# Kernel optimization log

Hardware: AMD Instinct MI355X
Metric: run time of the kernel (lower is better)

The kernel has to match this reference:

```python
import jax, jax.numpy as jnp
import numpy as np

N_NODES = 50000
N_EDGES = 800000
D = 128
H = 8
DH = D // H  # 16


def setup_inputs() -> dict:
    key = jax.random.key(0)
    ks = jax.random.split(key, 9)
    x = jax.random.normal(ks[0], (N_NODES, D), dtype=jnp.float32)
    # guarantee every node has >=1 incoming edge (avoids z == 0)
    dst_rand = jax.random.randint(ks[1], (N_EDGES - N_NODES,), 0, N_NODES, dtype=jnp.int64 if jax.config.jax_enable_x64 else jnp.int32)
    dst = jnp.concatenate([jnp.arange(N_NODES, dtype=dst_rand.dtype), dst_rand])
    src = jax.random.randint(ks[2], (N_EDGES,), 0, N_NODES, dtype=dst.dtype)
    scale = 0.05
    Wq = jax.random.normal(ks[3], (D, D), dtype=jnp.float32) * scale
    Wk = jax.random.normal(ks[4], (D, D), dtype=jnp.float32) * scale
    Wv = jax.random.normal(ks[5], (D, D), dtype=jnp.float32) * scale
    bq = jax.random.normal(ks[6], (D,), dtype=jnp.float32) * scale
    bk = jax.random.normal(ks[7], (D,), dtype=jnp.float32) * scale
    bv = jax.random.normal(ks[8], (D,), dtype=jnp.float32) * scale
    return {"x": x, "src": src, "dst": dst, "Wq": Wq, "bq": bq, "Wk": Wk, "bk": bk, "Wv": Wv, "bv": bv}


def reference(x, src, dst, Wq, bq, Wk, bk, Wv, bv):
    N = x.shape[0]
    # node projections -> [N, H, DH]
    Q = (x @ Wq + bq).reshape(N, H, DH)
    K = (x @ Wk + bk).reshape(N, H, DH)
    V = (x @ Wv + bv).reshape(N, H, DH)
    scale_const = jnp.sqrt(jnp.float32(DH))
    # per-edge score: (K[src] . Q[dst]) per head, then exp-clamp  -> [E, H]
    score = jnp.einsum('ehd,ehd->eh', K[src], Q[dst])
    score = jnp.exp(jnp.clip(score / scale_const, -5.0, 5.0))
    # scatter-sum by destination node
    wV = jax.ops.segment_sum(score[:, :, None] * V[src], dst, num_segments=N)  # [N,H,DH]
    z = jax.ops.segment_sum(score, dst, num_segments=N)  # [N,H]
    attn = (wV / z[:, :, None]).reshape(N, H * DH)
    # dropout p=0 -> identity; residual
    return x + attn
```

## Files before the change

### kernel.cpp

```cpp
#include <hip/hip_runtime.h>
#include <hip/hip_bf16.h>

#define N_NODES 50000
#define N_EDGES 800000
#define D 128
#define H 8

#define PROJ_BLOCKS ((N_NODES + 63) / 64)
#define HIST_BLOCKS 1024
#define SCAN_T 1024
#define PER_T 50

typedef __attribute__((ext_vector_type(8))) short short8;
typedef __attribute__((ext_vector_type(4))) float floatx4;

__device__ __forceinline__ float bfbits2f(unsigned short u) {
    union { unsigned int i; float f; } c; c.i = ((unsigned int)u) << 16; return c.f;
}
__device__ __forceinline__ unsigned short f2bfbits(float f) {
    __hip_bfloat16 h = __float2bfloat16(f);
    return *reinterpret_cast<unsigned short*>(&h);
}

__global__ __launch_bounds__(256) void prep_w_kernel(
    const float* __restrict__ Wq, const float* __restrict__ Wk,
    const float* __restrict__ Wv, __hip_bfloat16* __restrict__ Wt,
    int* __restrict__ counts)
{
    const int i = blockIdx.x * 256 + threadIdx.x;
    if (i < N_NODES) counts[i] = 0;
    if (i >= 3 * D * D) return;
    const int p = i >> 14;
    const int r = i & (D * D - 1);
    const int col = r >> 7;
    const int k = r & (D - 1);
    const float* W = (p == 0) ? Wq : (p == 1) ? Wk : Wv;
    Wt[i] = __float2bfloat16(W[k * D + col]);
}

__global__ __launch_bounds__(256) void proj_hist_kernel(
    const float* __restrict__ x,
    const __hip_bfloat16* __restrict__ Wt,
    const float* __restrict__ bq, const float* __restrict__ bk,
    const float* __restrict__ bv,
    unsigned short* __restrict__ Qb,
    unsigned int* __restrict__ KVi,
    const int* __restrict__ dst, int* __restrict__ counts)
{
    const int tid = threadIdx.x;

    if (blockIdx.x >= PROJ_BLOCKS) {
        const int i = (blockIdx.x - PROJ_BLOCKS) * 256 + tid;
        const int stride = HIST_BLOCKS * 256;
        for (int e = i; e < N_EDGES; e += stride)
            atomicAdd(&counts[dst[e]], 1);
        return;
    }

    const int m0   = blockIdx.x * 64;
    const int lane = tid & 63;
    const int wv   = tid >> 6;
    const int cb   = wv * 32;
    const int lr   = lane & 15;
    const int hi   = lane >> 4;

    __shared__ short xs[64][136];

    {
        const int row = tid >> 2;
        const int c0  = (tid & 3) * 32;
        int n = m0 + row; if (n >= N_NODES) n = N_NODES - 1;
        const float* xr = x + (size_t)n * D + c0;
        #pragma unroll
        for (int i = 0; i < 8; ++i) {
            const float4 f = *(const float4*)(xr + i * 4);
            short4 s;
            s.x = (short)f2bfbits(f.x); s.y = (short)f2bfbits(f.y);
            s.z = (short)f2bfbits(f.z); s.w = (short)f2bfbits(f.w);
            *(short4*)(&xs[row][c0 + i * 4]) = s;
        }
    }
    __syncthreads();

    floatx4 acc[3][4][2];
    #pragma unroll
    for (int p = 0; p < 3; ++p)
        #pragma unroll
        for (int rt = 0; rt < 4; ++rt)
            #pragma unroll
            for (int ct = 0; ct < 2; ++ct)
                acc[p][rt][ct] = (floatx4){0.f, 0.f, 0.f, 0.f};

    const short* Wts = (const short*)Wt;

    #pragma unroll
    for (int ks = 0; ks < 4; ++ks) {
        const int k0 = ks * 32 + hi * 8;

        short8 bfr[3][2];
        #pragma unroll
        for (int p = 0; p < 3; ++p)
            #pragma unroll
            for (int ct = 0; ct < 2; ++ct) {
                const int col = cb + ct * 16 + lr;
                bfr[p][ct] = *(const short8*)(Wts + ((size_t)(p * D + col) * D + k0));
            }

        short8 afr[4];
        #pragma unroll
        for (int rt = 0; rt < 4; ++rt)
            afr[rt] = *(const short8*)(&xs[rt * 16 + lr][k0]);

        #pragma unroll
        for (int p = 0; p < 3; ++p)
            #pragma unroll
            for (int ct = 0; ct < 2; ++ct)
                #pragma unroll
                for (int rt = 0; rt < 4; ++rt)
                    acc[p][rt][ct] = __builtin_amdgcn_mfma_f32_16x16x32_bf16(
                        afr[rt], bfr[p][ct], acc[p][rt][ct], 0, 0, 0);
    }

    #pragma unroll
    for (int ct = 0; ct < 2; ++ct) {
        const int col = cb + ct * 16 + lr;
        const float bkv = bk[col], bvv = bv[col];
        #pragma unroll
        for (int rt = 0; rt < 4; ++rt) {
            const int node0 = m0 + rt * 16 + hi * 4;
            if (node0 < N_NODES) {
                #pragma unroll
                for (int r = 0; r < 4; ++r) {
                    const unsigned int kk = f2bfbits(acc[1][rt][ct][r] + bkv);
                    const unsigned int vv = f2bfbits(acc[2][rt][ct][r] + bvv);
                    KVi[(size_t)(node0 + r) * 128 + col] = kk | (vv << 16);
                }
            }
        }
    }

    __syncthreads();
    #pragma unroll
    for (int ct = 0; ct < 2; ++ct) {
        const int col = cb + ct * 16 + lr;
        const float bqv = bq[col];
        #pragma unroll
        for (int rt = 0; rt < 4; ++rt) {
            const int nloc = rt * 16 + hi * 4;
            #pragma unroll
            for (int r = 0; r < 4; ++r)
                xs[nloc + r][col] = (short)f2bfbits(acc[0][rt][ct][r] + bqv);
        }
    }
    __syncthreads();
    {
        const int row = tid >> 2;
        const int c0  = (tid & 3) * 32;
        const int n   = m0 + row;
        if (n < N_NODES) {
            int4* dstp = (int4*)(Qb + (size_t)n * D + c0);
            const int4* srcp = (const int4*)(&xs[row][c0]);
            #pragma unroll
            for (int i = 0; i < 4; ++i) dstp[i] = srcp[i];
        }
    }
}

__global__ __launch_bounds__(SCAN_T) void scan_kernel(
    const int* __restrict__ counts, int* __restrict__ row_ptr,
    int* __restrict__ cursor)
{
    __shared__ int wsum[16];
    const int tid  = threadIdx.x;
    const int base = tid * PER_T;

    int tot = 0;
    if (tid < 1000) {
        #pragma unroll 10
        for (int j = 0; j < PER_T; ++j) tot += counts[base + j];
    }

    int incl = tot;
    #pragma unroll
    for (int off = 1; off < 64; off <<= 1) {
        const int v = __shfl_up(incl, off);
        if ((tid & 63) >= off) incl += v;
    }
    if ((tid & 63) == 63) wsum[tid >> 6] = incl;
    __syncthreads();
    if (tid == 0) {
        int run = 0;
        #pragma unroll
        for (int w = 0; w < 16; ++w) { const int v = wsum[w]; wsum[w] = run; run += v; }
    }
    __syncthreads();

    if (tid < 1000) {
        int run = (incl - tot) + wsum[tid >> 6];
        #pragma unroll 10
        for (int j = 0; j < PER_T; ++j) {
            const int c = counts[base + j];
            row_ptr[base + j] = run;
            cursor[base + j]  = run;
            run += c;
        }
    }
    if (tid == 0) row_ptr[N_NODES] = N_EDGES;
}

__global__ __launch_bounds__(256) void scatter_kernel(
    const int* __restrict__ dst, const int* __restrict__ src,
    int* __restrict__ cursor, int* __restrict__ srcs)
{
    const int i = blockIdx.x * blockDim.x + threadIdx.x;
    const int stride = gridDim.x * blockDim.x;
    for (int e = i; e < N_EDGES; e += stride) {
        const int pos = atomicAdd(&cursor[dst[e]], 1);
        srcs[pos] = src[e];
    }
}

__global__ __launch_bounds__(256) void aggregate_kernel(
    const int* __restrict__ row_ptr, const int* __restrict__ srcs,
    const unsigned short* __restrict__ Qb, const unsigned int* __restrict__ KVi,
    const float* __restrict__ x, float* __restrict__ out)
{
    const int lane = threadIdx.x & 63;
    const int t    = (blockIdx.x * blockDim.x + threadIdx.x) >> 6;
    if (t >= N_NODES) return;

    const unsigned int qbits = *(const unsigned int*)(Qb + (size_t)t * D + 2 * lane);
    const float q0 = bfbits2f((unsigned short)(qbits & 0xffff));
    const float q1 = bfbits2f((unsigned short)(qbits >> 16));

    int i = row_ptr[t];
    const int rp1 = row_ptr[t + 1];

    float accx = 0.f, accy = 0.f, zh = 0.f;
    const unsigned long long* KVs = (const unsigned long long*)KVi;

    for (; i + 4 <= rp1; i += 4) {
        const int s0 = srcs[i + 0];
        const int s1 = srcs[i + 1];
        const int s2 = srcs[i + 2];
        const int s3 = srcs[i + 3];
        const unsigned long long kv0 = KVs[(size_t)s0 * 64 + lane];
        const unsigned long long kv1 = KVs[(size_t)s1 * 64 + lane];
        const unsigned long long kv2 = KVs[(size_t)s2 * 64 + lane];
        const unsigned long long kv3 = KVs[(size_t)s3 * 64 + lane];

        float p0 = bfbits2f((unsigned short)kv0) * q0 + bfbits2f((unsigned short)(kv0 >> 32)) * q1;
        float p1 = bfbits2f((unsigned short)kv1) * q0 + bfbits2f((unsigned short)(kv1 >> 32)) * q1;
        float p2 = bfbits2f((unsigned short)kv2) * q0 + bfbits2f((unsigned short)(kv2 >> 32)) * q1;
        float p3 = bfbits2f((unsigned short)kv3) * q0 + bfbits2f((unsigned short)(kv3 >> 32)) * q1;

        p0 += __shfl_xor(p0, 1); p1 += __shfl_xor(p1, 1);
        p2 += __shfl_xor(p2, 1); p3 += __shfl_xor(p3, 1);
        p0 += __shfl_xor(p0, 2); p1 += __shfl_xor(p1, 2);
        p2 += __shfl_xor(p2, 2); p3 += __shfl_xor(p3, 2);
        p0 += __shfl_xor(p0, 4); p1 += __shfl_xor(p1, 4);
        p2 += __shfl_xor(p2, 4); p3 += __shfl_xor(p3, 4);

        const float w0 = __expf(fminf(fmaxf(p0 * 0.25f, -5.0f), 5.0f));
        const float w1 = __expf(fminf(fmaxf(p1 * 0.25f, -5.0f), 5.0f));
        const float w2 = __expf(fminf(fmaxf(p2 * 0.25f, -5.0f), 5.0f));
        const float w3 = __expf(fminf(fmaxf(p3 * 0.25f, -5.0f), 5.0f));

        accx += w0 * bfbits2f((unsigned short)(kv0 >> 16)) + w1 * bfbits2f((unsigned short)(kv1 >> 16))
              + w2 * bfbits2f((unsigned short)(kv2 >> 16)) + w3 * bfbits2f((unsigned short)(kv3 >> 16));
        accy += w0 * bfbits2f((unsigned short)(kv0 >> 48)) + w1 * bfbits2f((unsigned short)(kv1 >> 48))
              + w2 * bfbits2f((unsigned short)(kv2 >> 48)) + w3 * bfbits2f((unsigned short)(kv3 >> 48));
        zh   += (w0 + w1) + (w2 + w3);
    }
    for (; i < rp1; ++i) {
        const int s = srcs[i];
        const unsigned long long kv = KVs[(size_t)s * 64 + lane];
        float p = bfbits2f((unsigned short)kv) * q0 + bfbits2f((unsigned short)(kv >> 32)) * q1;
        p += __shfl_xor(p, 1);
        p += __shfl_xor(p, 2);
        p += __shfl_xor(p, 4);
        const float w = __expf(fminf(fmaxf(p * 0.25f, -5.0f), 5.0f));
        accx += w * bfbits2f((unsigned short)(kv >> 16));
        accy += w * bfbits2f((unsigned short)(kv >> 48));
        zh   += w;
    }

    const float inv = 1.0f / zh;
    const int base = t * D + 2 * lane;
    out[base + 0] = x[base + 0] + accx * inv;
    out[base + 1] = x[base + 1] + accy * inv;
}

extern "C" void kernel_launch(void* const* d_in, const int* in_sizes, int n_in,
                              void* d_out, int out_size, void* d_ws, size_t ws_size,
                              hipStream_t stream) {
    const float* x   = (const float*)d_in[0];
    const int*   src = (const int*)d_in[1];
    const int*   dst = (const int*)d_in[2];
    const float* Wq  = (const float*)d_in[3];
    const float* bq  = (const float*)d_in[4];
    const float* Wk  = (const float*)d_in[5];
    const float* bk  = (const float*)d_in[6];
    const float* Wv  = (const float*)d_in[7];
    const float* bv  = (const float*)d_in[8];

    unsigned short* Qb  = (unsigned short*)d_ws;
    unsigned int*   KVi = (unsigned int*)(Qb + (size_t)N_NODES * D);
    __hip_bfloat16* Wt  = (__hip_bfloat16*)(KVi + (size_t)N_NODES * 128);
    int* counts   = (int*)(Wt + 3 * D * D);
    int* row_ptr  = counts + 50048;
    int* cursor   = row_ptr + 50048;
    int* srcs     = cursor + 50048;

    float* out = (float*)d_out;

    prep_w_kernel<<<196, 256, 0, stream>>>(Wq, Wk, Wv, Wt, counts);

    proj_hist_kernel<<<PROJ_BLOCKS + HIST_BLOCKS, 256, 0, stream>>>(
        x, Wt, bq, bk, bv, Qb, KVi, dst, counts);

    scan_kernel<<<1, SCAN_T, 0, stream>>>(counts, row_ptr, cursor);

    scatter_kernel<<<1024, 256, 0, stream>>>(dst, src, cursor, srcs);

    aggregate_kernel<<<(N_NODES * 64 + 255) / 256, 256, 0, stream>>>(
        row_ptr, srcs, Qb, KVi, x, out);
}
```

Measured before the change: 275.6 us.

## Fuse preprocessing, projection, histogram, scan and scatter into one cooperative kernel

Replaces the four preprocessing launches (weight prep, projection+histogram, single-block scan, scatter) with one cooperative kernel that separates the phases with grid-wide syncs. The scan becomes a parallel two-level scan across 512 blocks instead of a single 1024-thread block, and each projection block now handles two 64-row tiles. The aim is to remove launch gaps and the serial single-block scan bottleneck, at the cost of grid.sync overhead and fewer blocks for projection and histogram work. A fallback to the old multi-kernel path is kept for when cooperative launch is unavailable.

```diff
diff --git a/kernel.cpp b/kernel.cpp
--- a/kernel.cpp
+++ b/kernel.cpp
@@ -1,13 +1,17 @@
 #include <hip/hip_runtime.h>
 #include <hip/hip_bf16.h>
+#include <hip/hip_cooperative_groups.h>
+
+namespace cg = cooperative_groups;
 
 #define N_NODES 50000
 #define N_EDGES 800000
 #define D 128
-#define H 8
-
-#define PROJ_BLOCKS ((N_NODES + 63) / 64)
-#define HIST_BLOCKS 1024
+
+#define COOP_BLOCKS 512
+#define PROJ_SPLIT  391
+#define HIST_BLOCKS (COOP_BLOCKS - PROJ_SPLIT)
+#define CHUNK 98
 #define SCAN_T 1024
 #define PER_T 50
 
@@ -22,49 +26,21 @@
     return *reinterpret_cast<unsigned short*>(&h);
 }
 
-__global__ __launch_bounds__(256) void prep_w_kernel(
-    const float* __restrict__ Wq, const float* __restrict__ Wk,
-    const float* __restrict__ Wv, __hip_bfloat16* __restrict__ Wt,
-    int* __restrict__ counts)
-{
-    const int i = blockIdx.x * 256 + threadIdx.x;
-    if (i < N_NODES) counts[i] = 0;
-    if (i >= 3 * D * D) return;
-    const int p = i >> 14;
-    const int r = i & (D * D - 1);
-    const int col = r >> 7;
-    const int k = r & (D - 1);
-    const float* W = (p == 0) ? Wq : (p == 1) ? Wk : Wv;
-    Wt[i] = __float2bfloat16(W[k * D + col]);
-}
-
-__global__ __launch_bounds__(256) void proj_hist_kernel(
-    const float* __restrict__ x,
-    const __hip_bfloat16* __restrict__ Wt,
+__device__ __forceinline__ void proj_tile(
+    const int m0, const int tid,
+    const float* __restrict__ x, const short* __restrict__ Wts,
     const float* __restrict__ bq, const float* __restrict__ bk,
     const float* __restrict__ bv,
-    unsigned short* __restrict__ Qb,
-    unsigned int* __restrict__ KVi,
-    const int* __restrict__ dst, int* __restrict__ counts)
-{
-    const int tid = threadIdx.x;
-
-    if (blockIdx.x >= PROJ_BLOCKS) {
-        const int i = (blockIdx.x - PROJ_BLOCKS) * 256 + tid;
-        const int stride = HIST_BLOCKS * 256;
-        for (int e = i; e < N_EDGES; e += stride)
-            atomicAdd(&counts[dst[e]], 1);
-        return;
-    }
-
-    const int m0   = blockIdx.x * 64;
+    unsigned short* __restrict__ Qb, unsigned int* __restrict__ KVi,
+    short (*xs)[136])
+{
     const int lane = tid & 63;
     const int wv   = tid >> 6;
     const int cb   = wv * 32;
     const int lr   = lane & 15;
     const int hi   = lane >> 4;
 
-    __shared__ short xs[64][136];
+    __syncthreads();
 
     {
         const int row = tid >> 2;
@@ -91,12 +67,9 @@
             for (int ct = 0; ct < 2; ++ct)
                 acc[p][rt][ct] = (floatx4){0.f, 0.f, 0.f, 0.f};
 
-    const short* Wts = (const short*)Wt;
-
     #pragma unroll
     for (int ks = 0; ks < 4; ++ks) {
         const int k0 = ks * 32 + hi * 8;
-
         short8 bfr[3][2];
         #pragma unroll
         for (int p = 0; p < 3; ++p)
@@ -105,7 +78,6 @@
                 const int col = cb + ct * 16 + lr;
                 bfr[p][ct] = *(const short8*)(Wts + ((size_t)(p * D + col) * D + k0));
             }
-
         short8 afr[4];
         #pragma unroll
         for (int rt = 0; rt < 4; ++rt)
@@ -166,6 +138,151 @@
     }
 }
 
+__device__ __forceinline__ void hist_loop(
+    const int rel_bid, const int nblocks, const int tid,
+    const int* __restrict__ dst, int* __restrict__ counts)
+{
+    const int i0 = rel_bid * 256 + tid;
+    const int stride = nblocks * 256;
+    for (int e = i0; e < N_EDGES; e += stride)
+        atomicAdd(&counts[dst[e]], 1);
+}
+
+__global__ __launch_bounds__(256, 2) void build_kernel(
+    const float* __restrict__ x,
+    const int* __restrict__ src, const int* __restrict__ dst,
+    const float* __restrict__ Wq, const float* __restrict__ bq,
+    const float* __restrict__ Wk, const float* __restrict__ bk,
+    const float* __restrict__ Wv, const float* __restrict__ bv,
+    __hip_bfloat16* __restrict__ Wt,
+    unsigned short* __restrict__ Qb, unsigned int* __restrict__ KVi,
+    int* __restrict__ counts, int* __restrict__ row_ptr,
+    int* __restrict__ cursor, int* __restrict__ blksum,
+    int* __restrict__ srcs)
+{
+    cg::grid_group grid = cg::this_grid();
+    const int tid  = threadIdx.x;
+    const int bid  = blockIdx.x;
+    const int gtid = bid * 256 + tid;
+
+    __shared__ short xs[64][136];
+    __shared__ int aux[4];
+
+    if (gtid < N_NODES) counts[gtid] = 0;
+    if (gtid < 3 * D * D) {
+        const int p = gtid >> 14;
+        const int r = gtid & (D * D - 1);
+        const int col = r >> 7;
+        const int k = r & (D - 1);
+        const float* W = (p == 0) ? Wq : (p == 1) ? Wk : Wv;
+        Wt[gtid] = __float2bfloat16(W[k * D + col]);
+    }
+    __threadfence();
+    grid.sync();
+
+    if (bid < PROJ_SPLIT) {
+        const short* Wts = (const short*)Wt;
+        proj_tile(bid * 2 * 64,       tid, x, Wts, bq, bk, bv, Qb, KVi, xs);
+        proj_tile((bid * 2 + 1) * 64, tid, x, Wts, bq, bk, bv, Qb, KVi, xs);
+    } else {
+        hist_loop(bid - PROJ_SPLIT, HIST_BLOCKS, tid, dst, counts);
+    }
+    __threadfence();
+    grid.sync();
+
+    {
+        int* sd = (int*)xs;
+        const int base = bid * CHUNK;
+        int v = 0;
+        if (tid < 128) {
+            if (tid < CHUNK) {
+                const int idx = base + tid;
+                if (idx < N_NODES) v = counts[idx];
+            }
+            sd[tid] = v;
+        }
+        __syncthreads();
+        #pragma unroll
+        for (int off = 1; off < 128; off <<= 1) {
+            int t = 0;
+            if (tid < 128 && tid >= off) t = sd[tid - off];
+            __syncthreads();
+            if (tid < 128) sd[tid] += t;
+            __syncthreads();
+        }
+        if (tid < CHUNK) {
+            const int idx = base + tid;
+            if (idx < N_NODES) row_ptr[idx] = sd[tid] - v;
+        }
+        if (tid == 127) blksum[bid] = sd[127];
+    }
+    __threadfence();
+    grid.sync();
+
+    {
+        int part = 0;
+        for (int j = tid; j < bid; j += 256) part += blksum[j];
+        #pragma unroll
+        for (int off = 32; off > 0; off >>= 1) part += __shfl_down(part, off);
+        if ((tid & 63) == 0) aux[tid >> 6] = part;
+        __syncthreads();
+        const int off4 = aux[0] + aux[1] + aux[2] + aux[3];
+
+        const int base = bid * CHUNK;
+        if (tid < CHUNK) {
+            const int idx = base + tid;
+            if (idx < N_NODES) {
+                const int rp = row_ptr[idx] + off4;
+                row_ptr[idx] = rp;
+                cursor[idx]  = rp;
+            }
+        }
+        if (bid == COOP_BLOCKS - 1 && tid == 0) row_ptr[N_NODES] = N_EDGES;
+    }
+    __threadfence();
+    grid.sync();
+
+    for (int e = gtid; e < N_EDGES; e += COOP_BLOCKS * 256) {
+        const int pos = atomicAdd(&cursor[dst[e]], 1);
+        srcs[pos] = src[e];
+    }
+}
+
+__global__ __launch_bounds__(256) void prep_w_kernel(
+    const float* __restrict__ Wq, const float* __restrict__ Wk,
+    const float* __restrict__ Wv, __hip_bfloat16* __restrict__ Wt,
+    int* __restrict__ counts)
+{
+    const int i = blockIdx.x * 256 + threadIdx.x;
+    if (i < N_NODES) counts[i] = 0;
+    if (i >= 3 * D * D) return;
+    const int p = i >> 14;
+    const int r = i & (D * D - 1);
+    const int col = r >> 7;
+    const int k = r & (D - 1);
+    const float* W = (p == 0) ? Wq : (p == 1) ? Wk : Wv;
+    Wt[i] = __float2bfloat16(W[k * D + col]);
+}
+
+__global__ __launch_bounds__(256) void proj_hist_kernel(
+    const float* __restrict__ x,
+    const __hip_bfloat16* __restrict__ Wt,
+    const float* __restrict__ bq, const float* __restrict__ bk,
+    const float* __restrict__ bv,
+    unsigned short* __restrict__ Qb, unsigned int* __restrict__ KVi,
+    const int* __restrict__ dst, int* __restrict__ counts)
+{
+    const int tid = threadIdx.x;
+    __shared__ short xs[64][136];
+    if (blockIdx.x < PROJ_SPLIT) {
+        const short* Wts = (const short*)Wt;
+        proj_tile(blockIdx.x * 2 * 64,       tid, x, Wts, bq, bk, bv, Qb, KVi, xs);
+        proj_tile((blockIdx.x * 2 + 1) * 64, tid, x, Wts, bq, bk, bv, Qb, KVi, xs);
+    } else {
+        hist_loop(blockIdx.x - PROJ_SPLIT, HIST_BLOCKS, tid, dst, counts);
+    }
+}
+
 __global__ __launch_bounds__(SCAN_T) void scan_kernel(
     const int* __restrict__ counts, int* __restrict__ row_ptr,
     int* __restrict__ cursor)
@@ -179,7 +296,6 @@
         #pragma unroll 10
         for (int j = 0; j < PER_T; ++j) tot += counts[base + j];
     }
-
     int incl = tot;
     #pragma unroll
     for (int off = 1; off < 64; off <<= 1) {
@@ -194,7 +310,6 @@
         for (int w = 0; w < 16; ++w) { const int v = wsum[w]; wsum[w] = run; run += v; }
     }
     __syncthreads();
-
     if (tid < 1000) {
         int run = (incl - tot) + wsum[tid >> 6];
         #pragma unroll 10
@@ -310,18 +425,36 @@
     int* counts   = (int*)(Wt + 3 * D * D);
     int* row_ptr  = counts + 50048;
     int* cursor   = row_ptr + 50048;
-    int* srcs     = cursor + 50048;
+    int* blksum   = cursor + 50048;
+    int* srcs     = blksum + 512;
 
     float* out = (float*)d_out;
 
-    prep_w_kernel<<<196, 256, 0, stream>>>(Wq, Wk, Wv, Wt, counts);
-
-    proj_hist_kernel<<<PROJ_BLOCKS + HIST_BLOCKS, 256, 0, stream>>>(
-        x, Wt, bq, bk, bv, Qb, KVi, dst, counts);
-
-    scan_kernel<<<1, SCAN_T, 0, stream>>>(counts, row_ptr, cursor);
-
-    scatter_kernel<<<1024, 256, 0, stream>>>(dst, src, cursor, srcs);
+    int occ = 0;
+    hipError_t oe = hipOccupancyMaxActiveBlocksPerMultiprocessor(
+        &occ, build_kernel, 256, 0);
+    bool coop_ok = (oe == hipSuccess) && (occ >= 2);
+
+    if (coop_ok) {
+        void* args[] = {
+            (void*)&x, (void*)&src, (void*)&dst,
+            (void*)&Wq, (void*)&bq, (void*)&Wk, (void*)&bk, (void*)&Wv, (void*)&bv,
+            (void*)&Wt, (void*)&Qb, (void*)&KVi,
+            (void*)&counts, (void*)&row_ptr, (void*)&cursor, (void*)&blksum,
+            (void*)&srcs
+        };
+        hipError_t le = hipLaunchCooperativeKernel(
+            (void*)build_kernel, dim3(COOP_BLOCKS), dim3(256), args, 0, stream);
+        if (le != hipSuccess) coop_ok = false;
+    }
+
+    if (!coop_ok) {
+        prep_w_kernel<<<196, 256, 0, stream>>>(Wq, Wk, Wv, Wt, counts);
+        proj_hist_kernel<<<PROJ_SPLIT + HIST_BLOCKS, 256, 0, stream>>>(
+            x, Wt, bq, bk, bv, Qb, KVi, dst, counts);
+        scan_kernel<<<1, SCAN_T, 0, stream>>>(counts, row_ptr, cursor);
+        scatter_kernel<<<1024, 256, 0, stream>>>(dst, src, cursor, srcs);
+    }
 
     aggregate_kernel<<<(N_NODES * 64 + 255) / 256, 256, 0, stream>>>(
         row_ptr, srcs, Qb, KVi, x, out);
```

Result: no change. 280.3 us (+1.7%).
